# Kernel tuning notes

Hardware: AMD Instinct MI355X
Metric: run time of the kernel (lower is better)

## Reference

```python
import jax, jax.numpy as jnp
import numpy as np

NUM_HEADS = 16
DIM_HEADS = 64
DIM_INPUT = 1024
DIM = NUM_HEADS * DIM_HEADS  # 1024


def setup_inputs() -> dict:
    key = jax.random.key(0)
    ks = jax.random.split(key, 8)
    B, S = 2, 2048
    inputs = jax.random.normal(ks[0], (B, S, DIM_INPUT), dtype=jnp.float32)
    attention_mask = jnp.zeros((B, 1, 1, S), dtype=jnp.float32)
    s = 1.0 / np.sqrt(DIM_INPUT)
    Wq = jax.random.normal(ks[1], (DIM_INPUT, DIM), dtype=jnp.float32) * s
    bq = jnp.zeros((DIM,), dtype=jnp.float32)
    Wk = jax.random.normal(ks[2], (DIM_INPUT, DIM), dtype=jnp.float32) * s
    bk = jnp.zeros((DIM,), dtype=jnp.float32)
    Wv = jax.random.normal(ks[3], (DIM_INPUT, DIM), dtype=jnp.float32) * s
    bv = jnp.zeros((DIM,), dtype=jnp.float32)
    return {"inputs": inputs, "attention_mask": attention_mask,
            "Wq": Wq, "bq": bq, "Wk": Wk, "bk": bk, "Wv": Wv, "bv": bv}


def _split_heads(x):
    # [B, S, H*dh] -> [B, H, S, dh]
    B, S, _ = x.shape
    return x.reshape(B, S, NUM_HEADS, DIM_HEADS).transpose(0, 2, 1, 3)


def reference(inputs, attention_mask, Wq, bq, Wk, bk, Wv, bv):
    q = _split_heads(inputs @ Wq + bq)  # [B,H,S,dh]
    k = _split_heads(inputs @ Wk + bk)
    v = _split_heads(inputs @ Wv + bv)
    scores = jnp.einsum('bhsd,bhtd->bhst', q, k) / np.sqrt(DIM_HEADS).astype(np.float32)
    scores = scores + attention_mask  # broadcast additive mask
    probs = jax.nn.softmax(scores, axis=-1)  # dropout is identity in eval
    ctx = jnp.einsum('bhst,bhtd->bhsd', probs, v)  # [B,H,S,dh]
    B, H, S, dh = ctx.shape
    return ctx.transpose(0, 2, 1, 3).reshape(B, S, H * dh)
```

## Files before the change

### kernel.cpp

```cpp
#include <hip/hip_runtime.h>


typedef __attribute__((ext_vector_type(4))) float f32x4;
typedef __attribute__((ext_vector_type(16))) float f32x16;
typedef __attribute__((ext_vector_type(8))) __bf16 bf16x8;

#define DEV static __device__ __forceinline__

constexpr int S_ = 2048;
constexpr int H_ = 16;
constexpr int DH_ = 64;
constexpr int M_ = 2 * S_;
constexpr int N3_ = 3 * 1024;
constexpr int K_ = 1024;
constexpr float LOG2E = 1.44269504088896340736f;

DEV unsigned short f2bf(float f) {
  unsigned u = __builtin_bit_cast(unsigned, f);
  u += 0x7fffu + ((u >> 16) & 1u);
  return (unsigned short)(u >> 16);
}

DEV unsigned cvt_pk(float lo, float hi) {
  unsigned d;
  asm("v_cvt_pk_bf16_f32 %0, %1, %2" : "=v"(d) : "v"(lo), "v"(hi));
  return d;
}

DEV void gload_lds16(const void* g, void* l) {
  __builtin_amdgcn_global_load_lds(
      (const __attribute__((address_space(1))) unsigned int*)g,
      (__attribute__((address_space(3))) unsigned int*)l, 16, 0, 0);
}

DEV int kswz(int row, int colb) { return row * 128 + (colb ^ ((row & 7) << 4)); }

__global__ __launch_bounds__(256) void prep(
    const float* __restrict__ X, const float* __restrict__ Wq,
    const float* __restrict__ Wk, const float* __restrict__ Wv,
    unsigned short* __restrict__ Xbf, unsigned short* __restrict__ Wt) {
  __shared__ float tile[32][33];
  const int id = blockIdx.x;
  const int tid = threadIdx.x;
  if (id < 3072) {
    int z = id >> 10, rem = id & 1023;
    const float* W = (z == 0) ? Wq : (z == 1) ? Wk : Wv;
    int n0 = (rem & 31) * 32, k0 = (rem >> 5) * 32;
    int tx = tid & 31, ty = tid >> 5;
    for (int i = 0; i < 4; ++i)
      tile[ty + i * 8][tx] = W[(size_t)(k0 + ty + i * 8) * 1024 + n0 + tx];
    __syncthreads();
    for (int i = 0; i < 4; ++i)
      Wt[(size_t)(z * 1024 + n0 + ty + i * 8) * 1024 + k0 + tx] =
          f2bf(tile[tx][ty + i * 8]);
  } else {
    int idx = ((id - 3072) * 256 + tid) * 8;
    float4 a = *(const float4*)(X + idx);
    float4 b = *(const float4*)(X + idx + 4);
    unsigned short r[8];
    r[0] = f2bf(a.x); r[1] = f2bf(a.y); r[2] = f2bf(a.z); r[3] = f2bf(a.w);
    r[4] = f2bf(b.x); r[5] = f2bf(b.y); r[6] = f2bf(b.z); r[7] = f2bf(b.w);
    *(uint4*)(Xbf + idx) = *(uint4*)r;
  }
}

__global__ __launch_bounds__(256, 2) void qkv_gemm(
    const unsigned short* __restrict__ Xbf, const unsigned short* __restrict__ Wt,
    const float* __restrict__ bq, const float* __restrict__ bk,
    const float* __restrict__ bv, unsigned short* __restrict__ Qw,
    unsigned short* __restrict__ Kw, unsigned short* __restrict__ Vt) {
  __shared__ unsigned short Abuf[128 * 64];
  __shared__ unsigned short Bbuf[128 * 64];
  int tid = threadIdx.x;
  int w = tid >> 6, l = tid & 63;
  int row16 = l & 15, kg = l >> 4;
  int mBase = blockIdx.y * 128, nBase = blockIdx.x * 128;
  int wm = w >> 1, wn = w & 1;

  f32x4 acc[4][4] = {};

  const int grow = l >> 3;
  const int gcol = ((l & 7) ^ grow) * 8;

  for (int kt = 0; kt < K_ / 64; ++kt) {
    int k0 = kt * 64;
    __syncthreads();
#pragma unroll
    for (int j = 0; j < 4; ++j) {
      int c1k = w * 4 + j;
      int r = c1k * 8 + grow;
      gload_lds16(Xbf + (size_t)(mBase + r) * K_ + k0 + gcol,
                  (char*)Abuf + c1k * 1024);
      gload_lds16(Wt + (size_t)(nBase + r) * K_ + k0 + gcol,
                  (char*)Bbuf + c1k * 1024);
    }
    __syncthreads();
#pragma unroll
    for (int kk = 0; kk < 2; ++kk) {
      bf16x8 af[4], bfr[4];
#pragma unroll
      for (int m = 0; m < 4; ++m)
        af[m] = *(const bf16x8*)((const char*)Abuf +
                 kswz(wm * 64 + m * 16 + row16, kk * 64 + kg * 16));
#pragma unroll
      for (int n = 0; n < 4; ++n)
        bfr[n] = *(const bf16x8*)((const char*)Bbuf +
                  kswz(wn * 64 + n * 16 + row16, kk * 64 + kg * 16));
#pragma unroll
      for (int m = 0; m < 4; ++m)
#pragma unroll
        for (int n = 0; n < 4; ++n)
          acc[m][n] = __builtin_amdgcn_mfma_f32_16x16x32_bf16(af[m], bfr[n],
                                                              acc[m][n], 0, 0, 0);
    }
  }

#pragma unroll
  for (int n = 0; n < 4; ++n) {
    int gn = nBase + wn * 64 + n * 16 + row16;
    int which = gn >> 10;
    int nn = gn & 1023;
    float bias = (which == 0 ? bq : which == 1 ? bk : bv)[nn];
    unsigned short* dst = (which == 0) ? Qw : (which == 1) ? Kw : Vt;
    float scl = (which == 0) ? 0.125f * LOG2E : 1.0f;
    int hh = nn >> 6, dd = nn & 63;
#pragma unroll
    for (int m = 0; m < 4; ++m) {
      int gm0 = mBase + wm * 64 + m * 16 + kg * 4;
#pragma unroll
      for (int j = 0; j < 4; ++j) {
        int gm = gm0 + j;
        int bb = gm >> 11, ss = gm & 2047;
        float v = (acc[m][n][j] + bias) * scl;
        size_t idx;
        if (which == 2)
          idx = ((size_t)(bb * H_ + hh) * DH_ + dd) * S_ + ss;
        else
          idx = ((size_t)(bb * H_ + hh) * S_ + ss) * DH_ + dd;
        dst[idx] = f2bf(v);
      }
    }
  }
}

__global__ __launch_bounds__(512, 4) void attn_fwd(
    const unsigned short* __restrict__ Qw, const unsigned short* __restrict__ Kw,
    const unsigned short* __restrict__ Vt, const float* __restrict__ mask,
    float* __restrict__ out) {
  __shared__ __align__(16) char LDS[73728];

  const int tid = threadIdx.x;
  const int w = tid >> 6, l = tid & 63;
  const int qg = w >> 1, thalf = w & 1;
  const int lq = l & 31;
  const int h = l >> 5;
  const int wgid = blockIdx.x;
  const int xcd = wgid & 7, ixd = wgid >> 3;
  const int bh = xcd + 8 * (ixd >> 4);
  const int qt = ixd & 15;
  const int b = bh >> 4, hh = bh & 15;
  const int q0 = qt * 128 + qg * 32;

  const unsigned short* Kb = Kw + (size_t)bh * S_ * DH_;
  const unsigned short* Vb = Vt + (size_t)bh * DH_ * S_;

  {
    float4 mv = *(const float4*)(mask + (size_t)b * S_ + tid * 4);
    mv.x *= LOG2E; mv.y *= LOG2E; mv.z *= LOG2E; mv.w *= LOG2E;
    *(float4*)(LDS + tid * 16) = mv;
  }

  bf16x8 qf[4];
  {
    const unsigned short* qrow = Qw + ((size_t)bh * S_ + q0 + lq) * DH_;
#pragma unroll
    for (int kk = 0; kk < 4; ++kk)
      qf[kk] = *(const bf16x8*)(qrow + kk * 16 + h * 8);
  }

  int rb[4];
#pragma unroll
  for (int kk = 0; kk < 4; ++kk)
    rb[kk] = 8192 + thalf * 8192 + lq * 128 + ((kk * 32 + h * 16) ^ ((lq & 7) << 4));
  const int srow = tid >> 3;
  const int tc8 = (tid & 7) * 8;
  const int wb = 8192 + srow * 128 + (((tid & 7) * 16) ^ ((srow & 7) << 4));
  const int mb = thalf * 256 + h * 16;

  bf16x8 kr[2], vr[2];
#pragma unroll
  for (int j = 0; j < 2; ++j) {
    kr[j] = *(const bf16x8*)(Kb + (size_t)(j * 64 + srow) * DH_ + tc8);
    vr[j] = *(const bf16x8*)(Vb + (size_t)srow * S_ + j * 64 + tc8);
  }
#pragma unroll
  for (int j = 0; j < 2; ++j) {
    *(bf16x8*)(LDS + wb + j * 8192) = kr[j];
    *(bf16x8*)(LDS + wb + 32768 + j * 8192) = vr[j];
  }
#pragma unroll
  for (int j = 0; j < 2; ++j) {
    kr[j] = *(const bf16x8*)(Kb + (size_t)(128 + j * 64 + srow) * DH_ + tc8);
    vr[j] = *(const bf16x8*)(Vb + (size_t)srow * S_ + 128 + j * 64 + tc8);
  }
  __syncthreads();

  float l_run = 0.f;
  f32x16 O0 = {}, O1 = {};

  auto body = [&](int p, int cur) __attribute__((always_inline)) {
    if (p < 15) {
#pragma unroll
      for (int j = 0; j < 2; ++j) {
        *(bf16x8*)(LDS + wb + j * 8192 + (cur ^ 1) * 16384) = kr[j];
        *(bf16x8*)(LDS + wb + 32768 + j * 8192 + (cur ^ 1) * 16384) = vr[j];
      }
      if (p < 14) {
        const int tn = (p + 2) * 128;
#pragma unroll
        for (int j = 0; j < 2; ++j) {
          kr[j] = *(const bf16x8*)(Kb + (size_t)(tn + j * 64 + srow) * DH_ + tc8);
          vr[j] = *(const bf16x8*)(Vb + (size_t)srow * S_ + tn + j * 64 + tc8);
        }
      }
    }

    const int mo = mb + p * 512;
    f32x16 p0, p1;
#pragma unroll
    for (int r2 = 0; r2 < 4; ++r2) {
      f32x4 a = *(const f32x4*)(LDS + mo + r2 * 32);
      f32x4 bq4 = *(const f32x4*)(LDS + mo + 128 + r2 * 32);
#pragma unroll
      for (int c = 0; c < 4; ++c) { p0[4 * r2 + c] = a[c]; p1[4 * r2 + c] = bq4[c]; }
    }

    __builtin_amdgcn_s_setprio(1);
#pragma unroll
    for (int kk = 0; kk < 4; ++kk) {
      bf16x8 kf0 = *(const bf16x8*)(LDS + rb[kk] + cur * 16384);
      bf16x8 kf1 = *(const bf16x8*)(LDS + rb[kk] + 4096 + cur * 16384);
      p0 = __builtin_amdgcn_mfma_f32_32x32x16_bf16(kf0, qf[kk], p0, 0, 0, 0);
      p1 = __builtin_amdgcn_mfma_f32_32x32x16_bf16(kf1, qf[kk], p1, 0, 0, 0);
    }
    __builtin_amdgcn_s_setprio(0);

#pragma unroll
    for (int i = 0; i < 16; ++i) {
      p0[i] = __builtin_amdgcn_exp2f(p0[i]);
      p1[i] = __builtin_amdgcn_exp2f(p1[i]);
    }

    float s8[8];
#pragma unroll
    for (int i = 0; i < 8; ++i)
      s8[i] = (p0[i] + p0[i + 8]) + (p1[i] + p1[i + 8]);
    float rs = ((s8[0] + s8[1]) + (s8[2] + s8[3])) +
               ((s8[4] + s8[5]) + (s8[6] + s8[7]));
    rs += __shfl_xor(rs, 32, 64);
    l_run += rs;

    unsigned w0[8], w1[8];
#pragma unroll
    for (int r2 = 0; r2 < 4; ++r2) {
      w0[2 * r2]     = cvt_pk(p0[4 * r2 + 0], p0[4 * r2 + 1]);
      w0[2 * r2 + 1] = cvt_pk(p0[4 * r2 + 2], p0[4 * r2 + 3]);
      w1[2 * r2]     = cvt_pk(p1[4 * r2 + 0], p1[4 * r2 + 1]);
      w1[2 * r2 + 1] = cvt_pk(p1[4 * r2 + 2], p1[4 * r2 + 3]);
    }

    __builtin_amdgcn_s_setprio(1);
#pragma unroll
    for (int s = 0; s < 4; ++s) {
      const unsigned* W = (s < 2) ? w0 : w1;
      const int base = (s & 1) * 4;
      unsigned send0 = h ? W[base + 0] : W[base + 2];
      unsigned send1 = h ? W[base + 1] : W[base + 3];
      unsigned c0 = (unsigned)__shfl_xor((int)send0, 32, 64);
      unsigned c1 = (unsigned)__shfl_xor((int)send1, 32, 64);
      uint4 fw;
      fw.x = h ? c0 : W[base + 0];
      fw.y = h ? c1 : W[base + 1];
      fw.z = h ? W[base + 2] : c0;
      fw.w = h ? W[base + 3] : c1;
      bf16x8 pf = __builtin_bit_cast(bf16x8, fw);
      bf16x8 vf0 = *(const bf16x8*)(LDS + rb[s] + 32768 + cur * 16384);
      O0 = __builtin_amdgcn_mfma_f32_32x32x16_bf16(vf0, pf, O0, 0, 0, 0);
      bf16x8 vf1 = *(const bf16x8*)(LDS + rb[s] + 36864 + cur * 16384);
      O1 = __builtin_amdgcn_mfma_f32_32x32x16_bf16(vf1, pf, O1, 0, 0, 0);
    }
    __builtin_amdgcn_s_setprio(0);

    __syncthreads();
  };

#pragma unroll 1
  for (int pp = 0; pp < 8; ++pp) {
    body(2 * pp, 0);
    body(2 * pp + 1, 1);
  }

  char* Osc = LDS + 8192;
  float* Mp = (float*)LDS;
  const int sbase = qg * 8192 + l * 128;
  const int sx = (l & 7) << 4;
  if (thalf == 1) {
#pragma unroll
    for (int i = 0; i < 4; ++i) {
      f32x4 v;
#pragma unroll
      for (int c = 0; c < 4; ++c) v[c] = O0[i * 4 + c];
      *(f32x4*)(Osc + sbase + ((i * 16) ^ sx)) = v;
    }
#pragma unroll
    for (int i = 0; i < 4; ++i) {
      f32x4 v;
#pragma unroll
      for (int c = 0; c < 4; ++c) v[c] = O1[i * 4 + c];
      *(f32x4*)(Osc + sbase + (((i + 4) * 16) ^ sx)) = v;
    }
    Mp[qg * 64 + l] = l_run;
  }
  __syncthreads();
  if (thalf == 0) {
#pragma unroll
    for (int i = 0; i < 4; ++i) {
      f32x4 v = *(const f32x4*)(Osc + sbase + ((i * 16) ^ sx));
#pragma unroll
      for (int c = 0; c < 4; ++c) O0[i * 4 + c] += v[c];
    }
#pragma unroll
    for (int i = 0; i < 4; ++i) {
      f32x4 v = *(const f32x4*)(Osc + sbase + (((i + 4) * 16) ^ sx));
#pragma unroll
      for (int c = 0; c < 4; ++c) O1[i * 4 + c] += v[c];
    }
    l_run += Mp[qg * 64 + l];

    float inv = 1.0f / l_run;
    float* orow = out + ((size_t)b * S_ + q0 + lq) * 1024 + hh * 64;
#pragma unroll
    for (int r2 = 0; r2 < 4; ++r2) {
      f32x4 v0, v1;
#pragma unroll
      for (int c = 0; c < 4; ++c) {
        v0[c] = O0[4 * r2 + c] * inv;
        v1[c] = O1[4 * r2 + c] * inv;
      }
      *(f32x4*)&orow[r2 * 8 + h * 4] = v0;
      *(f32x4*)&orow[32 + r2 * 8 + h * 4] = v1;
    }
  }
}

extern "C" void kernel_launch(void* const* d_in, const int* in_sizes, int n_in,
                              void* d_out, int out_size, void* d_ws, size_t ws_size,
                              hipStream_t stream) {
  const float* X = (const float*)d_in[0];
  const float* mask = (const float*)d_in[1];
  const float* Wq = (const float*)d_in[2];
  const float* bq = (const float*)d_in[3];
  const float* Wk = (const float*)d_in[4];
  const float* bk = (const float*)d_in[5];
  const float* Wv = (const float*)d_in[6];
  const float* bv = (const float*)d_in[7];
  float* out = (float*)d_out;

  char* ws = (char*)d_ws;
  unsigned short* Xbf = (unsigned short*)ws;
  unsigned short* Wt  = (unsigned short*)(ws + (size_t)(8 << 20));
  unsigned short* Qw  = (unsigned short*)(ws + (size_t)(14 << 20));
  unsigned short* Kw  = (unsigned short*)(ws + (size_t)(22 << 20));
  unsigned short* Vt  = (unsigned short*)(ws + (size_t)(30 << 20));

  prep<<<dim3(3072 + 2048), dim3(256), 0, stream>>>(X, Wq, Wk, Wv, Xbf, Wt);
  qkv_gemm<<<dim3(N3_ / 128, M_ / 128), dim3(256), 0, stream>>>(
      Xbf, Wt, bq, bk, bv, Qw, Kw, Vt);
  attn_fwd<<<dim3(512), dim3(512), 0, stream>>>(Qw, Kw, Vt, mask, out);
}
```

Before: 92.36 us.

## Halve attention workgroup size and drop LDS double buffering for occupancy

Workgroups in the attention kernel shrink from 512 to 256 threads, each covering 64 queries instead of 128, and the grid doubles to 1024. LDS drops to 40 KB by replacing the double-buffered K/V tiles with a single buffer that is written and synchronised at the start of each iteration, with register prefetch of the next tile. The row-sum shuffle is moved out of the loop and done once at the end. The aim is more resident workgroups per CU, but each iteration now carries an extra barrier and load/compute overlap is reduced. K/V tiles are also read from global memory twice as often across the grid.

Result: slower. 117.8 us (+27.5%).

```diff
diff --git a/kernel.cpp b/kernel.cpp
--- a/kernel.cpp
+++ b/kernel.cpp
@@ -143,11 +143,11 @@
   }
 }
 
-__global__ __launch_bounds__(512, 4) void attn_fwd(
+__global__ __launch_bounds__(256, 4) void attn_fwd(
     const unsigned short* __restrict__ Qw, const unsigned short* __restrict__ Kw,
     const unsigned short* __restrict__ Vt, const float* __restrict__ mask,
     float* __restrict__ out) {
-  __shared__ __align__(16) char LDS[73728];
+  __shared__ __align__(16) char LDS[40960];
 
   const int tid = threadIdx.x;
   const int w = tid >> 6, l = tid & 63;
@@ -156,18 +156,22 @@
   const int h = l >> 5;
   const int wgid = blockIdx.x;
   const int xcd = wgid & 7, ixd = wgid >> 3;
-  const int bh = xcd + 8 * (ixd >> 4);
-  const int qt = ixd & 15;
+  const int bh = xcd + 8 * (ixd >> 5);
+  const int qt = ixd & 31;
   const int b = bh >> 4, hh = bh & 15;
-  const int q0 = qt * 128 + qg * 32;
+  const int q0 = qt * 64 + qg * 32;
 
   const unsigned short* Kb = Kw + (size_t)bh * S_ * DH_;
   const unsigned short* Vb = Vt + (size_t)bh * DH_ * S_;
 
   {
-    float4 mv = *(const float4*)(mask + (size_t)b * S_ + tid * 4);
-    mv.x *= LOG2E; mv.y *= LOG2E; mv.z *= LOG2E; mv.w *= LOG2E;
-    *(float4*)(LDS + tid * 16) = mv;
+    const float* mrow = mask + (size_t)b * S_ + tid * 8;
+    float4 m0 = *(const float4*)mrow;
+    float4 m1 = *(const float4*)(mrow + 4);
+    m0.x *= LOG2E; m0.y *= LOG2E; m0.z *= LOG2E; m0.w *= LOG2E;
+    m1.x *= LOG2E; m1.y *= LOG2E; m1.z *= LOG2E; m1.w *= LOG2E;
+    *(float4*)(LDS + tid * 32) = m0;
+    *(float4*)(LDS + tid * 32 + 16) = m1;
   }
 
   bf16x8 qf[4];
@@ -181,51 +185,49 @@
   int rb[4];
 #pragma unroll
   for (int kk = 0; kk < 4; ++kk)
-    rb[kk] = 8192 + thalf * 8192 + lq * 128 + ((kk * 32 + h * 16) ^ ((lq & 7) << 4));
+    rb[kk] = 8192 + thalf * 8192 + lq * 128 +
+             ((kk * 32 + h * 16) ^ ((lq & 7) << 4));
+
   const int srow = tid >> 3;
-  const int tc8 = (tid & 7) * 8;
+  const int slot8 = (tid & 7) * 8;
   const int wb = 8192 + srow * 128 + (((tid & 7) * 16) ^ ((srow & 7) << 4));
-  const int mb = thalf * 256 + h * 16;
-
-  bf16x8 kr[2], vr[2];
-#pragma unroll
-  for (int j = 0; j < 2; ++j) {
-    kr[j] = *(const bf16x8*)(Kb + (size_t)(j * 64 + srow) * DH_ + tc8);
-    vr[j] = *(const bf16x8*)(Vb + (size_t)srow * S_ + j * 64 + tc8);
-  }
-#pragma unroll
-  for (int j = 0; j < 2; ++j) {
-    *(bf16x8*)(LDS + wb + j * 8192) = kr[j];
-    *(bf16x8*)(LDS + wb + 32768 + j * 8192) = vr[j];
-  }
-#pragma unroll
-  for (int j = 0; j < 2; ++j) {
-    kr[j] = *(const bf16x8*)(Kb + (size_t)(128 + j * 64 + srow) * DH_ + tc8);
-    vr[j] = *(const bf16x8*)(Vb + (size_t)srow * S_ + 128 + j * 64 + tc8);
-  }
+
+  bf16x8 kr[2][2], vr[2][2];
+#pragma unroll
+  for (int j = 0; j < 2; ++j)
+#pragma unroll
+    for (int i = 0; i < 2; ++i) {
+      kr[j][i] = *(const bf16x8*)(Kb + (size_t)(j * 64 + i * 32 + srow) * DH_ + slot8);
+      vr[j][i] = *(const bf16x8*)(Vb + (size_t)(i * 32 + srow) * S_ + j * 64 + slot8);
+    }
   __syncthreads();
 
-  float l_run = 0.f;
+  float l_acc = 0.f;
   f32x16 O0 = {}, O1 = {};
 
-  auto body = [&](int p, int cur) __attribute__((always_inline)) {
+#pragma unroll 1
+  for (int p = 0; p < 16; ++p) {
+#pragma unroll
+    for (int j = 0; j < 2; ++j) {
+      *(bf16x8*)(LDS + wb + j * 8192) = kr[j][0];
+      *(bf16x8*)(LDS + wb + 4096 + j * 8192) = kr[j][1];
+      *(bf16x8*)(LDS + wb + 16384 + j * 8192) = vr[j][0];
+      *(bf16x8*)(LDS + wb + 20480 + j * 8192) = vr[j][1];
+    }
+    __syncthreads();
+
     if (p < 15) {
-#pragma unroll
-      for (int j = 0; j < 2; ++j) {
-        *(bf16x8*)(LDS + wb + j * 8192 + (cur ^ 1) * 16384) = kr[j];
-        *(bf16x8*)(LDS + wb + 32768 + j * 8192 + (cur ^ 1) * 16384) = vr[j];
-      }
-      if (p < 14) {
-        const int tn = (p + 2) * 128;
-#pragma unroll
-        for (int j = 0; j < 2; ++j) {
-          kr[j] = *(const bf16x8*)(Kb + (size_t)(tn + j * 64 + srow) * DH_ + tc8);
-          vr[j] = *(const bf16x8*)(Vb + (size_t)srow * S_ + tn + j * 64 + tc8);
+      const int tn = (p + 1) * 128;
+#pragma unroll
+      for (int j = 0; j < 2; ++j)
+#pragma unroll
+        for (int i = 0; i < 2; ++i) {
+          kr[j][i] = *(const bf16x8*)(Kb + (size_t)(tn + j * 64 + i * 32 + srow) * DH_ + slot8);
+          vr[j][i] = *(const bf16x8*)(Vb + (size_t)(i * 32 + srow) * S_ + tn + j * 64 + slot8);
         }
-      }
-    }
-
-    const int mo = mb + p * 512;
+    }
+
+    const int mo = thalf * 256 + h * 16 + p * 512;
     f32x16 p0, p1;
 #pragma unroll
     for (int r2 = 0; r2 < 4; ++r2) {
@@ -238,8 +240,8 @@
     __builtin_amdgcn_s_setprio(1);
 #pragma unroll
     for (int kk = 0; kk < 4; ++kk) {
-      bf16x8 kf0 = *(const bf16x8*)(LDS + rb[kk] + cur * 16384);
-      bf16x8 kf1 = *(const bf16x8*)(LDS + rb[kk] + 4096 + cur * 16384);
+      bf16x8 kf0 = *(const bf16x8*)(LDS + rb[kk]);
+      bf16x8 kf1 = *(const bf16x8*)(LDS + rb[kk] + 4096);
       p0 = __builtin_amdgcn_mfma_f32_32x32x16_bf16(kf0, qf[kk], p0, 0, 0, 0);
       p1 = __builtin_amdgcn_mfma_f32_32x32x16_bf16(kf1, qf[kk], p1, 0, 0, 0);
     }
@@ -255,10 +257,8 @@
 #pragma unroll
     for (int i = 0; i < 8; ++i)
       s8[i] = (p0[i] + p0[i + 8]) + (p1[i] + p1[i + 8]);
-    float rs = ((s8[0] + s8[1]) + (s8[2] + s8[3])) +
-               ((s8[4] + s8[5]) + (s8[6] + s8[7]));
-    rs += __shfl_xor(rs, 32, 64);
-    l_run += rs;
+    l_acc += ((s8[0] + s8[1]) + (s8[2] + s8[3])) +
+             ((s8[4] + s8[5]) + (s8[6] + s8[7]));
 
     unsigned w0[8], w1[8];
 #pragma unroll
@@ -284,21 +284,17 @@
       fw.z = h ? W[base + 2] : c0;
       fw.w = h ? W[base + 3] : c1;
       bf16x8 pf = __builtin_bit_cast(bf16x8, fw);
-      bf16x8 vf0 = *(const bf16x8*)(LDS + rb[s] + 32768 + cur * 16384);
+      bf16x8 vf0 = *(const bf16x8*)(LDS + rb[s] + 16384);
       O0 = __builtin_amdgcn_mfma_f32_32x32x16_bf16(vf0, pf, O0, 0, 0, 0);
-      bf16x8 vf1 = *(const bf16x8*)(LDS + rb[s] + 36864 + cur * 16384);
+      bf16x8 vf1 = *(const bf16x8*)(LDS + rb[s] + 20480);
       O1 = __builtin_amdgcn_mfma_f32_32x32x16_bf16(vf1, pf, O1, 0, 0, 0);
     }
     __builtin_amdgcn_s_setprio(0);
 
     __syncthreads();
-  };
-
-#pragma unroll 1
-  for (int pp = 0; pp < 8; ++pp) {
-    body(2 * pp, 0);
-    body(2 * pp + 1, 1);
-  }
+  }
+
+  float l_run = l_acc + __shfl_xor(l_acc, 32, 64);
 
   char* Osc = LDS + 8192;
   float* Mp = (float*)LDS;
@@ -376,5 +372,5 @@
   prep<<<dim3(3072 + 2048), dim3(256), 0, stream>>>(X, Wq, Wk, Wv, Xbf, Wt);
   qkv_gemm<<<dim3(N3_ / 128, M_ / 128), dim3(256), 0, stream>>>(
       Xbf, Wt, bq, bk, bv, Qw, Kw, Vt);
-  attn_fwd<<<dim3(512), dim3(512), 0, stream>>>(Qw, Kw, Vt, mask, out);
-}
+  attn_fwd<<<dim3(1024), dim3(256), 0, stream>>>(Qw, Kw, Vt, mask, out);
+}
```
